# Kernel tuning notes

Hardware: AMD Instinct MI355X
Metric: run time of the kernel (lower is better)

Reference implementation:

```python
import jax, jax.numpy as jnp
import numpy as np

GROUPS = 32
EPS = 1e-6


def group_norm(x, gamma, beta):
    # x: [B, C, T], normalize per group of channels over (C//G, T)
    B, C, T = x.shape
    xr = x.reshape(B, GROUPS, C // GROUPS, T)
    mean = xr.mean(axis=(2, 3), keepdims=True)
    var = xr.var(axis=(2, 3), keepdims=True)
    xn = ((xr - mean) * jax.lax.rsqrt(var + EPS)).reshape(B, C, T)
    return xn * gamma[None, :, None] + beta[None, :, None]


def conv1x1(h, w, b):
    # 1x1 Conv1d == channel matmul. h: [B,C,T], w: [O,C], b: [O]
    return jnp.einsum('oc,bct->bot', w, h) + b[None, :, None]


def setup_inputs() -> dict:
    key = jax.random.key(0)
    ks = jax.random.split(key, 10)
    B, C, T = 8, 512, 2048
    s = 1.0 / np.sqrt(C)
    return {
        'x': jax.random.normal(ks[0], (B, C, T), jnp.float32),
        'gamma': jnp.ones((C,), jnp.float32),
        'beta': jnp.zeros((C,), jnp.float32),
        'q_w': jax.random.normal(ks[1], (C, C), jnp.float32) * s,
        'q_b': jnp.zeros((C,), jnp.float32),
        'k_w': jax.random.normal(ks[2], (C, C), jnp.float32) * s,
        'k_b': jnp.zeros((C,), jnp.float32),
        'v_w': jax.random.normal(ks[3], (C, C), jnp.float32) * s,
        'v_b': jnp.zeros((C,), jnp.float32),
        'o_w': jax.random.normal(ks[4], (C, C), jnp.float32) * s,
        'o_b': jnp.zeros((C,), jnp.float32),
    }


def reference(x, gamma, beta, q_w, q_b, k_w, k_b, v_w, v_b, o_w, o_b):
    h = group_norm(x, gamma, beta)
    q = conv1x1(h, q_w, q_b)  # [B,C,T]
    k = conv1x1(h, k_w, k_b)
    v = conv1x1(h, v_w, v_b)
    B, C, T = q.shape
    scale = jnp.asarray(C, q.dtype) ** -0.5
    # scores[b,t,s] = sum_c q[b,c,t] * k[b,c,s]
    scores = jnp.einsum('bct,bcs->bts', q, k) * scale
    w = jax.nn.softmax(scores, axis=-1)
    # out[b,c,t] = sum_s v[b,c,s] * w[b,t,s]
    h = jnp.einsum('bcs,bts->bct', v, w)
    h = conv1x1(h, o_w, o_b)
    return x + h
```

## Files before the change

kernel.cpp:

```cpp
#include <hip/hip_runtime.h>
#include <hip/hip_bf16.h>
#include <stdint.h>

typedef __bf16 bf16_t;
typedef __attribute__((ext_vector_type(8))) __bf16 bf16x8;
typedef __attribute__((ext_vector_type(4))) __bf16 bf16x4;
typedef __attribute__((ext_vector_type(4))) float f32x4;

__device__ __forceinline__ bool is_fp32(const void* gamma) {
  return ((const unsigned*)gamma)[0] == 0x3F800000u;
}

__device__ __forceinline__ void async_copy16(const bf16_t* g, bf16_t* l) {
  __builtin_amdgcn_global_load_lds(
      (const __attribute__((address_space(1))) void*)g,
      (__attribute__((address_space(3))) void*)l, 16, 0, 0);
}

#define GFENCE() asm volatile("" ::: "memory")

__device__ __forceinline__ void hard_barrier() {
  GFENCE();
  __builtin_amdgcn_sched_barrier(0);
  __builtin_amdgcn_s_barrier();
  __builtin_amdgcn_sched_barrier(0);
  GFENCE();
}

template <int NW>
__device__ __forceinline__ void vm_wait() {
  if constexpr (NW == 8)
    asm volatile("s_waitcnt vmcnt(8)" ::: "memory");
  else if constexpr (NW == 6)
    asm volatile("s_waitcnt vmcnt(6)" ::: "memory");
  else
    asm volatile("s_waitcnt vmcnt(0)" ::: "memory");
}

__global__ __launch_bounds__(256) void prepass(
    const void* __restrict__ q_w, const void* __restrict__ k_w,
    const void* __restrict__ v_w, const void* __restrict__ o_w,
    const void* __restrict__ gamma, const void* __restrict__ beta,
    const void* __restrict__ q_b, const void* __restrict__ k_b,
    const void* __restrict__ v_b, const void* __restrict__ o_b,
    const void* __restrict__ xv, bf16_t* __restrict__ wdst,
    bf16_t* __restrict__ vdst, float* __restrict__ rowsum,
    float* __restrict__ stats) {
  const bool fp32 = is_fp32(gamma);
  int bid = blockIdx.x;
  int tid = threadIdx.x;
  if (bid < 4172) {
    int i = bid * 256 + tid;
    if (i < 1048576) {
      const void* wsrc[4] = {q_w, k_w, v_w, o_w};
      int seg = i >> 18, off = i & 262143;
      const void* s = wsrc[seg];
      wdst[i] = fp32 ? (bf16_t)((const float*)s)[off] : ((const bf16_t*)s)[off];
    } else {
      int j = i - 1048576;
      if (j < 3072) {
        const void* vsrc[6] = {gamma, beta, q_b, k_b, v_b, o_b};
        int seg = j >> 9, off = j & 511;
        const void* s = vsrc[seg];
        vdst[j] =
            fp32 ? (bf16_t)((const float*)s)[off] : ((const bf16_t*)s)[off];
      } else {
        int j2 = j - 3072;
        if (j2 < 16384) rowsum[j2] = 0.0f;
      }
    }
    return;
  }
  int gidx = bid - 4172;
  long long base = (long long)gidx * 16 * 2048;
  float s = 0.f, q = 0.f;
#pragma unroll
  for (int ch = 0; ch < 16; ++ch) {
    long long off = base + (long long)ch * 2048 + tid * 8;
    float f[8];
    if (fp32) {
      const float* xf = (const float*)xv;
      float4 u = *(const float4*)(xf + off);
      float4 w = *(const float4*)(xf + off + 4);
      f[0] = u.x; f[1] = u.y; f[2] = u.z; f[3] = u.w;
      f[4] = w.x; f[5] = w.y; f[6] = w.z; f[7] = w.w;
    } else {
      bf16x8 vv = *(const bf16x8*)((const bf16_t*)xv + off);
#pragma unroll
      for (int e = 0; e < 8; ++e) f[e] = (float)vv[e];
    }
#pragma unroll
    for (int e = 0; e < 8; ++e) {
      s += f[e];
      q += f[e] * f[e];
    }
  }
  for (int o = 32; o > 0; o >>= 1) {
    s += __shfl_down(s, o);
    q += __shfl_down(q, o);
  }
  __shared__ float red[8];
  int wave = tid >> 6, lane = tid & 63;
  if (lane == 0) {
    red[wave] = s;
    red[4 + wave] = q;
  }
  __syncthreads();
  if (tid == 0) {
    stats[gidx * 2 + 0] = red[0] + red[1] + red[2] + red[3];
    stats[gidx * 2 + 1] = red[4] + red[5] + red[6] + red[7];
  }
}

__global__ __launch_bounds__(256) void gn_apply(const void* __restrict__ xv,
                                                const float* __restrict__ stats,
                                                const bf16_t* __restrict__ gammab,
                                                const bf16_t* __restrict__ betab,
                                                bf16_t* __restrict__ ht,
                                                const void* __restrict__ gamma) {
  const int C = 512, T = 2048;
  const bool fp32 = is_fp32(gamma);
  int bid = blockIdx.x;
  int ts = bid & 3;
  int gp = (bid >> 2) & 15;
  int b = bid >> 6;
  int tid = threadIdx.x;
  int c0 = gp * 32;
  int t0 = ts * 512;
  int cw = tid & 31;
  int gloc = cw >> 4;
  int gidx = b * 32 + gp * 2 + gloc;
  const float inv = 1.0f / 32768.0f;
  float mean = stats[gidx * 2] * inv;
  float var = stats[gidx * 2 + 1] * inv - mean * mean;
  float rstd = rsqrtf(var + 1e-6f);
  float sc = rstd * (float)gammab[c0 + cw];
  float sh = (float)betab[c0 + cw] - mean * sc;

  __shared__ bf16_t tile[32 * 68];
  const float* xf = (const float*)xv;
  const bf16_t* xb = (const bf16_t*)xv;
  long long xbase = ((long long)b * C + c0) * T + t0;
  bf16_t* hb = ht + ((long long)b * T + t0) * C + c0;
  for (int ch = 0; ch < 8; ++ch) {
    if (fp32) {
#pragma unroll
      for (int p = 0; p < 2; ++p) {
        int e = p * 256 + tid;
        int c = e >> 4, t = (e & 15) * 4;
        long long off = xbase + (long long)c * T + ch * 64 + t;
        float4 u = *(const float4*)(xf + off);
        bf16x4 w;
        w[0] = (bf16_t)u.x; w[1] = (bf16_t)u.y;
        w[2] = (bf16_t)u.z; w[3] = (bf16_t)u.w;
        *(bf16x4*)&tile[c * 68 + t] = w;
      }
    } else {
      int c = tid >> 3, t = (tid & 7) * 8;
      long long off = xbase + (long long)c * T + ch * 64 + t;
      bf16x8 u = *(const bf16x8*)(xb + off);
      bf16x4 lo, hi;
#pragma unroll
      for (int e = 0; e < 4; ++e) { lo[e] = u[e]; hi[e] = u[e + 4]; }
      *(bf16x4*)&tile[c * 68 + t] = lo;
      *(bf16x4*)&tile[c * 68 + t + 4] = hi;
    }
    __syncthreads();
#pragma unroll
    for (int s2 = 0; s2 < 8; ++s2) {
      int t = s2 * 8 + (tid >> 5);
      float v = (float)tile[cw * 68 + t];
      hb[(long long)(ch * 64 + t) * C + cw] = (bf16_t)(v * sc + sh);
    }
    __syncthreads();
  }
}

template <int BM, bool BIASM, bool BIASN, bool RESOUT, bool EXPSUM,
          bool NORMROW, int M, int N, int K, int LDA, int LDB, int LDC>
__device__ __forceinline__ void gemm8_body(
    const bf16_t* __restrict__ A, long long sA, const bf16_t* __restrict__ B,
    long long sB, void* __restrict__ Cout, long long sC,
    const bf16_t* __restrict__ biasM, const bf16_t* __restrict__ biasN,
    const void* __restrict__ Res, long long sR, float alpha,
    const void* __restrict__ gamma, float* __restrict__ rowsum, int m0, int n0,
    int b, bf16_t* lds) {
  constexpr int AI = BM / 32;
  constexpr int AR = BM * 32;
  constexpr int L = BM / 128 + 2;
  const int tid = threadIdx.x;
  const int lane = tid & 63;
  const int lane15 = lane & 15;
  const int quad = lane >> 4;
  const int wave = tid >> 6;
  const int wm = wave >> 2;
  const int wn = wave & 3;

  const bf16_t* Ab = A + (long long)b * sA + (long long)m0 * LDA;
  const bf16_t* Bb = B + (long long)b * sB + (long long)n0 * LDB;

  bf16_t* ldsA = lds;
  bf16_t* ldsB = lds + 4 * AR;

  const int srow = tid >> 2;
  const int sg = ((tid & 3) - (srow >> 1)) & 3;
  const bf16_t* As_src = Ab + (long long)srow * LDA + sg * 8;
  const bf16_t* Bs_src = Bb + (long long)srow * LDB + sg * 8;
  const long long A128 = 128LL * LDA, B128 = 128LL * LDB;

  auto stA = [&](int kelem, int r) {
    async_copy16(As_src + kelem, ldsA + r * AR + tid * 8);
    if constexpr (BM == 256)
      async_copy16(As_src + A128 + kelem, ldsA + r * AR + tid * 8 + 4096);
  };
  auto stB = [&](int kelem, int r) {
    async_copy16(Bs_src + kelem, ldsB + r * 8192 + tid * 8);
    async_copy16(Bs_src + B128 + kelem, ldsB + r * 8192 + tid * 8 + 4096);
  };

  const int slot = ((quad + (lane15 >> 1)) & 3) * 8;
  const int aoff = (wm * (BM / 2) + lane15) * 32 + slot;
  const int boff = (wn * 64 + lane15) * 32 + slot;

  bf16x8 af[AI];
  f32x4 acc[AI][4] = {};

  auto lda_frags = [&](int r) {
#pragma unroll
    for (int i = 0; i < AI; ++i)
      af[i] = *(const bf16x8*)(ldsA + r * AR + aoff + i * 512);
  };
  auto ldbf = [&](int r, int j) {
    return *(const bf16x8*)(ldsB + r * 8192 + boff + j * 512);
  };

  auto phaseA = [&](int rdA, int rdB, int stk, int str) {
    lda_frags(rdA);
    bf16x8 b0 = ldbf(rdB, 0), b1 = ldbf(rdB, 1);
    stA(stk, str);
    hard_barrier();
    asm volatile("s_waitcnt lgkmcnt(0)" ::: "memory");
    __builtin_amdgcn_sched_barrier(0);
    __builtin_amdgcn_s_setprio(1);
#pragma unroll
    for (int i = 0; i < AI; ++i) {
      acc[i][0] = __builtin_amdgcn_mfma_f32_16x16x32_bf16(af[i], b0, acc[i][0], 0, 0, 0);
      acc[i][1] = __builtin_amdgcn_mfma_f32_16x16x32_bf16(af[i], b1, acc[i][1], 0, 0, 0);
    }
    __builtin_amdgcn_s_setprio(0);
    hard_barrier();
  };
  auto phaseB = [&](int rdB, int stk, int str) {
    bf16x8 b0 = ldbf(rdB, 2), b1 = ldbf(rdB, 3);
    stB(stk, str);
    hard_barrier();
    asm volatile("s_waitcnt lgkmcnt(0)" ::: "memory");
    __builtin_amdgcn_sched_barrier(0);
    __builtin_amdgcn_s_setprio(1);
#pragma unroll
    for (int i = 0; i < AI; ++i) {
      acc[i][2] = __builtin_amdgcn_mfma_f32_16x16x32_bf16(af[i], b0, acc[i][2], 0, 0, 0);
      acc[i][3] = __builtin_amdgcn_mfma_f32_16x16x32_bf16(af[i], b1, acc[i][3], 0, 0, 0);
    }
    __builtin_amdgcn_s_setprio(0);
    vm_wait<2 * L>();
    hard_barrier();
  };

  const int NT = K / 64;
  const int NI = NT / 2;

  stA(0, 0);
  stB(0, 0);
  stA(32, 1);
  stB(32, 1);
  stA(64, 2);
  stB(64, 2);
  vm_wait<2 * L>();
  hard_barrier();

#pragma unroll 1
  for (int it = 0; it < NI; ++it) {
    const int ku = it * 128;
    const bool last = (it == NI - 1);
    const int ku2 = last ? 0 : ku + 128;
    const int kv2 = last ? 64 : ku + 192;
    phaseA(0, 0, ku + 96, 3);
    phaseB(0, ku + 96, 3);
    phaseA(1, 1, ku2, 0);
    phaseB(1, ku2, 0);
    phaseA(2, 2, ku2 + 32, 1);
    phaseB(2, ku2 + 32, 1);
    phaseA(3, 3, kv2, 2);
    phaseB(3, kv2, 2);
  }
  asm volatile("s_waitcnt vmcnt(0)" ::: "memory");

  if (EXPSUM) {
#pragma unroll
    for (int i = 0; i < AI; ++i) {
#pragma unroll
      for (int r = 0; r < 4; ++r) {
        long long m = m0 + wm * (BM / 2) + i * 16 + quad * 4 + r;
        float partial = 0.f;
#pragma unroll
        for (int j = 0; j < 4; ++j) {
          long long n = n0 + wn * 64 + j * 16 + lane15;
          float v = __expf(acc[i][j][r] * alpha);
          partial += v;
          ((bf16_t*)Cout)[(long long)b * sC + m * LDC + n] = (bf16_t)v;
        }
        partial += __shfl_xor(partial, 1);
        partial += __shfl_xor(partial, 2);
        partial += __shfl_xor(partial, 4);
        partial += __shfl_xor(partial, 8);
        if (lane15 == 0) atomicAdd(&rowsum[(long long)b * M + m], partial);
      }
    }
    return;
  }

  float invr[AI][4];
  if (NORMROW) {
#pragma unroll
    for (int i = 0; i < AI; ++i)
#pragma unroll
      for (int r = 0; r < 4; ++r)
        invr[i][r] = 1.0f / rowsum[(long long)b * M + m0 + wm * (BM / 2) +
                                   i * 16 + quad * 4 + r];
  }
  bool fp32 = false;
  if (RESOUT) fp32 = is_fp32(gamma);
#pragma unroll
  for (int i = 0; i < AI; ++i) {
#pragma unroll
    for (int j = 0; j < 4; ++j) {
#pragma unroll
      for (int r = 0; r < 4; ++r) {
        long long m = m0 + wm * (BM / 2) + i * 16 + quad * 4 + r;
        long long n = n0 + wn * 64 + j * 16 + lane15;
        float v = acc[i][j][r] * alpha;
        if (NORMROW) v *= invr[i][r];
        if (BIASM) v += (float)biasM[m];
        if (BIASN) v += (float)biasN[n];
        long long idx = (long long)b * sC + m * LDC + n;
        if (RESOUT) {
          long long ridx = (long long)b * sR + m * LDC + n;
          if (fp32) {
            v += ((const float*)Res)[ridx];
            ((float*)Cout)[idx] = v;
          } else {
            v += (float)((const bf16_t*)Res)[ridx];
            ((bf16_t*)Cout)[idx] = (bf16_t)v;
          }
        } else {
          ((bf16_t*)Cout)[idx] = (bf16_t)v;
        }
      }
    }
  }
}

__global__ __launch_bounds__(512, 2) void qkv_fat(
    const bf16_t* __restrict__ ht, const bf16_t* __restrict__ wqk,
    const bf16_t* __restrict__ wv, bf16_t* __restrict__ qkt,
    bf16_t* __restrict__ vvb, const bf16_t* __restrict__ qkb,
    const bf16_t* __restrict__ vbb, const void* __restrict__ gamma) {
  __shared__ __align__(16) bf16_t lds[65536];
  const long long TC = 2048LL * 512, CT = 512LL * 2048;
  int bid = blockIdx.x;
  if (bid < 256) {
    int b = bid >> 5, rem = bid & 31;
    int n0 = (rem & 3) * 256, m0 = (rem >> 2) * 256;
    gemm8_body<256, false, true, false, false, false, 2048, 1024, 512, 512,
               512, 1024>(ht, TC, wqk, 0, qkt, 2048LL * 1024, nullptr, qkb,
                          nullptr, 0, 1.0f, gamma, nullptr, m0, n0, b, lds);
  } else {
    int id2 = bid - 256;
    int b = id2 >> 5, rem = id2 & 31;
    int m0 = (rem & 3) * 128, n0 = (rem >> 2) * 256;
    gemm8_body<128, true, false, false, false, false, 512, 2048, 512, 512,
               512, 2048>(wv, 0, ht, TC, vvb, CT, vbb, nullptr, nullptr, 0,
                          1.0f, gamma, nullptr, m0, n0, b, lds);
  }
}

__global__ __launch_bounds__(512, 2) void scores_kernel(
    const bf16_t* __restrict__ qkt, bf16_t* __restrict__ Sm,
    const void* __restrict__ gamma, float* __restrict__ rowsum, float alpha) {
  __shared__ __align__(16) bf16_t lds[65536];
  int x = blockIdx.x;
  int gid = x >> 4, win = x & 15;
  int gm = gid & 1, gn = gid >> 1;
  int m0 = (gm * 4 + (win & 3)) * 256;
  int n0 = (gn * 4 + (win >> 2)) * 256;
  gemm8_body<256, false, false, false, true, false, 2048, 2048, 512, 1024,
             1024, 2048>(qkt, 2048LL * 1024, qkt + 512, 2048LL * 1024, Sm,
                         2048LL * 2048, nullptr, nullptr, nullptr, 0, alpha,
                         gamma, rowsum, m0, n0, blockIdx.z, lds);
}

__global__ __launch_bounds__(512, 2) void av_kernel(
    const bf16_t* __restrict__ Sm, const bf16_t* __restrict__ vvb,
    bf16_t* __restrict__ h2t, const void* __restrict__ gamma,
    float* __restrict__ rowsum) {
  __shared__ __align__(16) bf16_t lds[49152];
  gemm8_body<128, false, false, false, false, true, 2048, 512, 2048, 2048,
             2048, 512>(Sm, 2048LL * 2048, vvb, 512LL * 2048, h2t,
                        2048LL * 512, nullptr, nullptr, nullptr, 0, 1.0f,
                        gamma, rowsum, blockIdx.y * 128, blockIdx.x * 256,
                        blockIdx.z, lds);
}

__global__ __launch_bounds__(512, 2) void final_kernel(
    const bf16_t* __restrict__ wo, const bf16_t* __restrict__ h2t,
    void* __restrict__ out, const bf16_t* __restrict__ obb,
    const void* __restrict__ x, const void* __restrict__ gamma) {
  __shared__ __align__(16) bf16_t lds[49152];
  const long long TC = 2048LL * 512, CT = 512LL * 2048;
  gemm8_body<128, true, false, true, false, false, 512, 2048, 512, 512, 512,
             2048>(wo, 0, h2t, TC, out, CT, obb, nullptr, x, CT, 1.0f, gamma,
                   nullptr, blockIdx.y * 128, blockIdx.x * 256, blockIdx.z,
                   lds);
}

extern "C" void kernel_launch(void* const* d_in, const int* in_sizes, int n_in,
                              void* d_out, int out_size, void* d_ws,
                              size_t ws_size, hipStream_t stream) {
  const void* x = d_in[0];
  const void* gamma = d_in[1];
  const void* beta = d_in[2];
  const void* q_w = d_in[3];
  const void* q_b = d_in[4];
  const void* k_w = d_in[5];
  const void* k_b = d_in[6];
  const void* v_w = d_in[7];
  const void* v_b = d_in[8];
  const void* o_w = d_in[9];
  const void* o_b = d_in[10];

  const long long BTC = 8LL * 2048 * 512;
  char* ws = (char*)d_ws;
  float* stats = (float*)(ws + 256);
  bf16_t* wq = (bf16_t*)(ws + 4096);
  bf16_t* wv = wq + 2 * 262144;
  bf16_t* wo = wq + 3 * 262144;
  bf16_t* vdst = wq + 4 * 262144;
  bf16_t* gammab = vdst + 0 * 512;
  bf16_t* betab = vdst + 1 * 512;
  bf16_t* qkb = vdst + 2 * 512;
  bf16_t* vbb = vdst + 4 * 512;
  bf16_t* obb = vdst + 5 * 512;
  float* rowsum = (float*)(ws + 4096 + 2 * 1024 * 1024 + 8192);
  const size_t hdr = 4096 + 2 * 1024 * 1024 + 8192 + 65536;
  bf16_t* ht = (bf16_t*)(ws + hdr);
  bf16_t* vvb = ht + BTC;
  bf16_t* Sm = vvb + BTC;
  bf16_t* h2t = ht;
  bf16_t* qkt = (bf16_t*)d_out;

  const float scale = 0.044194173824159216f;

  prepass<<<4428, 256, 0, stream>>>(q_w, k_w, v_w, o_w, gamma, beta, q_b, k_b,
                                    v_b, o_b, x, wq, vdst, rowsum, stats);
  gn_apply<<<512, 256, 0, stream>>>(x, stats, gammab, betab, ht, gamma);
  qkv_fat<<<512, 512, 0, stream>>>(ht, wq, wv, qkt, vvb, qkb, vbb, gamma);
  scores_kernel<<<dim3(64, 1, 8), 512, 0, stream>>>(qkt, Sm, gamma, rowsum,
                                                    scale);
  av_kernel<<<dim3(2, 16, 8), 512, 0, stream>>>(Sm, vvb, h2t, gamma, rowsum);
  final_kernel<<<dim3(8, 4, 8), 512, 0, stream>>>(wo, h2t, d_out, obb, x,
                                                  gamma);
}
```

Measured before the change: 279.9 us.

## Fuse all stages into one cooperative persistent kernel with grid syncs

Replaces the six separate kernel launches with a single cooperative kernel of 256 blocks that runs prepass, group-norm apply, QKV, scores, AV and output projection as stages separated by grid.sync, with a multi-launch fallback. The GEMM body now loops over several tiles per block and prefetches the next tile's first k-slices during the last iteration, so one persistent block can cover more work. This removes launch gaps and tail effects between kernels. In exchange it fixes the grid at 256 blocks (about one per CU), which lowers occupancy, and it adds grid-wide barrier costs.

```diff
diff --git a/kernel.cpp b/kernel.cpp
--- a/kernel.cpp
+++ b/kernel.cpp
@@ -1,6 +1,9 @@
 #include <hip/hip_runtime.h>
+#include <hip/hip_cooperative_groups.h>
 #include <hip/hip_bf16.h>
 #include <stdint.h>
+
+namespace cg = cooperative_groups;
 
 typedef __bf16 bf16_t;
 typedef __attribute__((ext_vector_type(8))) __bf16 bf16x8;
@@ -37,154 +40,15 @@
     asm volatile("s_waitcnt vmcnt(0)" ::: "memory");
 }
 
-__global__ __launch_bounds__(256) void prepass(
-    const void* __restrict__ q_w, const void* __restrict__ k_w,
-    const void* __restrict__ v_w, const void* __restrict__ o_w,
-    const void* __restrict__ gamma, const void* __restrict__ beta,
-    const void* __restrict__ q_b, const void* __restrict__ k_b,
-    const void* __restrict__ v_b, const void* __restrict__ o_b,
-    const void* __restrict__ xv, bf16_t* __restrict__ wdst,
-    bf16_t* __restrict__ vdst, float* __restrict__ rowsum,
-    float* __restrict__ stats) {
-  const bool fp32 = is_fp32(gamma);
-  int bid = blockIdx.x;
-  int tid = threadIdx.x;
-  if (bid < 4172) {
-    int i = bid * 256 + tid;
-    if (i < 1048576) {
-      const void* wsrc[4] = {q_w, k_w, v_w, o_w};
-      int seg = i >> 18, off = i & 262143;
-      const void* s = wsrc[seg];
-      wdst[i] = fp32 ? (bf16_t)((const float*)s)[off] : ((const bf16_t*)s)[off];
-    } else {
-      int j = i - 1048576;
-      if (j < 3072) {
-        const void* vsrc[6] = {gamma, beta, q_b, k_b, v_b, o_b};
-        int seg = j >> 9, off = j & 511;
-        const void* s = vsrc[seg];
-        vdst[j] =
-            fp32 ? (bf16_t)((const float*)s)[off] : ((const bf16_t*)s)[off];
-      } else {
-        int j2 = j - 3072;
-        if (j2 < 16384) rowsum[j2] = 0.0f;
-      }
-    }
-    return;
-  }
-  int gidx = bid - 4172;
-  long long base = (long long)gidx * 16 * 2048;
-  float s = 0.f, q = 0.f;
-#pragma unroll
-  for (int ch = 0; ch < 16; ++ch) {
-    long long off = base + (long long)ch * 2048 + tid * 8;
-    float f[8];
-    if (fp32) {
-      const float* xf = (const float*)xv;
-      float4 u = *(const float4*)(xf + off);
-      float4 w = *(const float4*)(xf + off + 4);
-      f[0] = u.x; f[1] = u.y; f[2] = u.z; f[3] = u.w;
-      f[4] = w.x; f[5] = w.y; f[6] = w.z; f[7] = w.w;
-    } else {
-      bf16x8 vv = *(const bf16x8*)((const bf16_t*)xv + off);
-#pragma unroll
-      for (int e = 0; e < 8; ++e) f[e] = (float)vv[e];
-    }
-#pragma unroll
-    for (int e = 0; e < 8; ++e) {
-      s += f[e];
-      q += f[e] * f[e];
-    }
-  }
-  for (int o = 32; o > 0; o >>= 1) {
-    s += __shfl_down(s, o);
-    q += __shfl_down(q, o);
-  }
-  __shared__ float red[8];
-  int wave = tid >> 6, lane = tid & 63;
-  if (lane == 0) {
-    red[wave] = s;
-    red[4 + wave] = q;
-  }
-  __syncthreads();
-  if (tid == 0) {
-    stats[gidx * 2 + 0] = red[0] + red[1] + red[2] + red[3];
-    stats[gidx * 2 + 1] = red[4] + red[5] + red[6] + red[7];
-  }
-}
-
-__global__ __launch_bounds__(256) void gn_apply(const void* __restrict__ xv,
-                                                const float* __restrict__ stats,
-                                                const bf16_t* __restrict__ gammab,
-                                                const bf16_t* __restrict__ betab,
-                                                bf16_t* __restrict__ ht,
-                                                const void* __restrict__ gamma) {
-  const int C = 512, T = 2048;
-  const bool fp32 = is_fp32(gamma);
-  int bid = blockIdx.x;
-  int ts = bid & 3;
-  int gp = (bid >> 2) & 15;
-  int b = bid >> 6;
-  int tid = threadIdx.x;
-  int c0 = gp * 32;
-  int t0 = ts * 512;
-  int cw = tid & 31;
-  int gloc = cw >> 4;
-  int gidx = b * 32 + gp * 2 + gloc;
-  const float inv = 1.0f / 32768.0f;
-  float mean = stats[gidx * 2] * inv;
-  float var = stats[gidx * 2 + 1] * inv - mean * mean;
-  float rstd = rsqrtf(var + 1e-6f);
-  float sc = rstd * (float)gammab[c0 + cw];
-  float sh = (float)betab[c0 + cw] - mean * sc;
-
-  __shared__ bf16_t tile[32 * 68];
-  const float* xf = (const float*)xv;
-  const bf16_t* xb = (const bf16_t*)xv;
-  long long xbase = ((long long)b * C + c0) * T + t0;
-  bf16_t* hb = ht + ((long long)b * T + t0) * C + c0;
-  for (int ch = 0; ch < 8; ++ch) {
-    if (fp32) {
-#pragma unroll
-      for (int p = 0; p < 2; ++p) {
-        int e = p * 256 + tid;
-        int c = e >> 4, t = (e & 15) * 4;
-        long long off = xbase + (long long)c * T + ch * 64 + t;
-        float4 u = *(const float4*)(xf + off);
-        bf16x4 w;
-        w[0] = (bf16_t)u.x; w[1] = (bf16_t)u.y;
-        w[2] = (bf16_t)u.z; w[3] = (bf16_t)u.w;
-        *(bf16x4*)&tile[c * 68 + t] = w;
-      }
-    } else {
-      int c = tid >> 3, t = (tid & 7) * 8;
-      long long off = xbase + (long long)c * T + ch * 64 + t;
-      bf16x8 u = *(const bf16x8*)(xb + off);
-      bf16x4 lo, hi;
-#pragma unroll
-      for (int e = 0; e < 4; ++e) { lo[e] = u[e]; hi[e] = u[e + 4]; }
-      *(bf16x4*)&tile[c * 68 + t] = lo;
-      *(bf16x4*)&tile[c * 68 + t + 4] = hi;
-    }
-    __syncthreads();
-#pragma unroll
-    for (int s2 = 0; s2 < 8; ++s2) {
-      int t = s2 * 8 + (tid >> 5);
-      float v = (float)tile[cw * 68 + t];
-      hb[(long long)(ch * 64 + t) * C + cw] = (bf16_t)(v * sc + sh);
-    }
-    __syncthreads();
-  }
-}
-
-template <int BM, bool BIASM, bool BIASN, bool RESOUT, bool EXPSUM,
+template <int BM, int TCNT, bool BIASM, bool BIASN, bool RESOUT, bool EXPSUM,
           bool NORMROW, int M, int N, int K, int LDA, int LDB, int LDC>
 __device__ __forceinline__ void gemm8_body(
     const bf16_t* __restrict__ A, long long sA, const bf16_t* __restrict__ B,
     long long sB, void* __restrict__ Cout, long long sC,
     const bf16_t* __restrict__ biasM, const bf16_t* __restrict__ biasN,
     const void* __restrict__ Res, long long sR, float alpha,
-    const void* __restrict__ gamma, float* __restrict__ rowsum, int m0, int n0,
-    int b, bf16_t* lds) {
+    const void* __restrict__ gamma, float* __restrict__ rowsum,
+    const int* m0s, const int* n0s, int b, bf16_t* lds) {
   constexpr int AI = BM / 32;
   constexpr int AR = BM * 32;
   constexpr int L = BM / 128 + 2;
@@ -196,26 +60,21 @@
   const int wm = wave >> 2;
   const int wn = wave & 3;
 
-  const bf16_t* Ab = A + (long long)b * sA + (long long)m0 * LDA;
-  const bf16_t* Bb = B + (long long)b * sB + (long long)n0 * LDB;
-
   bf16_t* ldsA = lds;
   bf16_t* ldsB = lds + 4 * AR;
 
   const int srow = tid >> 2;
   const int sg = ((tid & 3) - (srow >> 1)) & 3;
-  const bf16_t* As_src = Ab + (long long)srow * LDA + sg * 8;
-  const bf16_t* Bs_src = Bb + (long long)srow * LDB + sg * 8;
   const long long A128 = 128LL * LDA, B128 = 128LL * LDB;
 
-  auto stA = [&](int kelem, int r) {
-    async_copy16(As_src + kelem, ldsA + r * AR + tid * 8);
+  auto stA = [&](const bf16_t* src, int kelem, int r) {
+    async_copy16(src + kelem, ldsA + r * AR + tid * 8);
     if constexpr (BM == 256)
-      async_copy16(As_src + A128 + kelem, ldsA + r * AR + tid * 8 + 4096);
+      async_copy16(src + A128 + kelem, ldsA + r * AR + tid * 8 + 4096);
   };
-  auto stB = [&](int kelem, int r) {
-    async_copy16(Bs_src + kelem, ldsB + r * 8192 + tid * 8);
-    async_copy16(Bs_src + B128 + kelem, ldsB + r * 8192 + tid * 8 + 4096);
+  auto stB = [&](const bf16_t* src, int kelem, int r) {
+    async_copy16(src + kelem, ldsB + r * 8192 + tid * 8);
+    async_copy16(src + B128 + kelem, ldsB + r * 8192 + tid * 8 + 4096);
   };
 
   const int slot = ((quad + (lane15 >> 1)) & 3) * 8;
@@ -223,7 +82,7 @@
   const int boff = (wn * 64 + lane15) * 32 + slot;
 
   bf16x8 af[AI];
-  f32x4 acc[AI][4] = {};
+  f32x4 acc[AI][4];
 
   auto lda_frags = [&](int r) {
 #pragma unroll
@@ -234,10 +93,10 @@
     return *(const bf16x8*)(ldsB + r * 8192 + boff + j * 512);
   };
 
-  auto phaseA = [&](int rdA, int rdB, int stk, int str) {
+  auto phaseA = [&](int rdA, int rdB, const bf16_t* src, int stk, int str) {
     lda_frags(rdA);
     bf16x8 b0 = ldbf(rdB, 0), b1 = ldbf(rdB, 1);
-    stA(stk, str);
+    stA(src, stk, str);
     hard_barrier();
     asm volatile("s_waitcnt lgkmcnt(0)" ::: "memory");
     __builtin_amdgcn_sched_barrier(0);
@@ -250,9 +109,9 @@
     __builtin_amdgcn_s_setprio(0);
     hard_barrier();
   };
-  auto phaseB = [&](int rdB, int stk, int str) {
+  auto phaseB = [&](int rdB, const bf16_t* src, int stk, int str) {
     bf16x8 b0 = ldbf(rdB, 2), b1 = ldbf(rdB, 3);
-    stB(stk, str);
+    stB(src, stk, str);
     hard_barrier();
     asm volatile("s_waitcnt lgkmcnt(0)" ::: "memory");
     __builtin_amdgcn_sched_barrier(0);
@@ -267,161 +126,386 @@
     hard_barrier();
   };
 
-  const int NT = K / 64;
-  const int NI = NT / 2;
-
-  stA(0, 0);
-  stB(0, 0);
-  stA(32, 1);
-  stB(32, 1);
-  stA(64, 2);
-  stB(64, 2);
-  vm_wait<2 * L>();
-  hard_barrier();
+  constexpr int NI = K / 128;
+
+#pragma unroll
+  for (int t = 0; t < TCNT; ++t) {
+    const int m0 = m0s[t], n0 = n0s[t];
+    const bf16_t* Acur = A + (long long)b * sA + (long long)m0 * LDA +
+                         (long long)srow * LDA + sg * 8;
+    const bf16_t* Bcur = B + (long long)b * sB + (long long)n0 * LDB +
+                         (long long)srow * LDB + sg * 8;
+    const int tn = (t + 1 < TCNT) ? t + 1 : t;
+    const bf16_t* Anxt = A + (long long)b * sA + (long long)m0s[tn] * LDA +
+                         (long long)srow * LDA + sg * 8;
+    const bf16_t* Bnxt = B + (long long)b * sB + (long long)n0s[tn] * LDB +
+                         (long long)srow * LDB + sg * 8;
+
+    if (t == 0) {
+      stA(Acur, 0, 0); stB(Bcur, 0, 0);
+      stA(Acur, 32, 1); stB(Bcur, 32, 1);
+      stA(Acur, 64, 2); stB(Bcur, 64, 2);
+      vm_wait<2 * L>();
+      hard_barrier();
+    }
+
+#pragma unroll
+    for (int i = 0; i < AI; ++i)
+#pragma unroll
+      for (int j = 0; j < 4; ++j) acc[i][j] = {0.f, 0.f, 0.f, 0.f};
 
 #pragma unroll 1
-  for (int it = 0; it < NI; ++it) {
-    const int ku = it * 128;
-    const bool last = (it == NI - 1);
-    const int ku2 = last ? 0 : ku + 128;
-    const int kv2 = last ? 64 : ku + 192;
-    phaseA(0, 0, ku + 96, 3);
-    phaseB(0, ku + 96, 3);
-    phaseA(1, 1, ku2, 0);
-    phaseB(1, ku2, 0);
-    phaseA(2, 2, ku2 + 32, 1);
-    phaseB(2, ku2 + 32, 1);
-    phaseA(3, 3, kv2, 2);
-    phaseB(3, kv2, 2);
-  }
-  asm volatile("s_waitcnt vmcnt(0)" ::: "memory");
-
-  if (EXPSUM) {
-#pragma unroll
-    for (int i = 0; i < AI; ++i) {
-#pragma unroll
-      for (int r = 0; r < 4; ++r) {
-        long long m = m0 + wm * (BM / 2) + i * 16 + quad * 4 + r;
-        float partial = 0.f;
-#pragma unroll
-        for (int j = 0; j < 4; ++j) {
-          long long n = n0 + wn * 64 + j * 16 + lane15;
-          float v = __expf(acc[i][j][r] * alpha);
-          partial += v;
-          ((bf16_t*)Cout)[(long long)b * sC + m * LDC + n] = (bf16_t)v;
-        }
-        partial += __shfl_xor(partial, 1);
-        partial += __shfl_xor(partial, 2);
-        partial += __shfl_xor(partial, 4);
-        partial += __shfl_xor(partial, 8);
-        if (lane15 == 0) atomicAdd(&rowsum[(long long)b * M + m], partial);
-      }
-    }
-    return;
-  }
-
-  float invr[AI][4];
-  if (NORMROW) {
-#pragma unroll
-    for (int i = 0; i < AI; ++i)
-#pragma unroll
-      for (int r = 0; r < 4; ++r)
-        invr[i][r] = 1.0f / rowsum[(long long)b * M + m0 + wm * (BM / 2) +
-                                   i * 16 + quad * 4 + r];
-  }
-  bool fp32 = false;
-  if (RESOUT) fp32 = is_fp32(gamma);
-#pragma unroll
-  for (int i = 0; i < AI; ++i) {
-#pragma unroll
-    for (int j = 0; j < 4; ++j) {
-#pragma unroll
-      for (int r = 0; r < 4; ++r) {
-        long long m = m0 + wm * (BM / 2) + i * 16 + quad * 4 + r;
-        long long n = n0 + wn * 64 + j * 16 + lane15;
-        float v = acc[i][j][r] * alpha;
-        if (NORMROW) v *= invr[i][r];
-        if (BIASM) v += (float)biasM[m];
-        if (BIASN) v += (float)biasN[n];
-        long long idx = (long long)b * sC + m * LDC + n;
-        if (RESOUT) {
-          long long ridx = (long long)b * sR + m * LDC + n;
-          if (fp32) {
-            v += ((const float*)Res)[ridx];
-            ((float*)Cout)[idx] = v;
-          } else {
-            v += (float)((const bf16_t*)Res)[ridx];
-            ((bf16_t*)Cout)[idx] = (bf16_t)v;
+    for (int it = 0; it < NI; ++it) {
+      const int ku = it * 128;
+      const bool lastit = (it == NI - 1);
+      const bf16_t* sAs = lastit ? Anxt : Acur;
+      const bf16_t* sBs = lastit ? Bnxt : Bcur;
+      const int k0n = lastit ? 0 : ku + 128;
+      const int k1n = lastit ? 32 : ku + 160;
+      const int k2n = lastit ? 64 : ku + 192;
+      phaseA(0, 0, Acur, ku + 96, 3);
+      phaseB(0, Bcur, ku + 96, 3);
+      phaseA(1, 1, sAs, k0n, 0);
+      phaseB(1, sBs, k0n, 0);
+      phaseA(2, 2, sAs, k1n, 1);
+      phaseB(2, sBs, k1n, 1);
+      phaseA(3, 3, sAs, k2n, 2);
+      phaseB(3, sBs, k2n, 2);
+    }
+    if (t == TCNT - 1) asm volatile("s_waitcnt vmcnt(0)" ::: "memory");
+
+    if constexpr (EXPSUM) {
+#pragma unroll
+      for (int i = 0; i < AI; ++i) {
+#pragma unroll
+        for (int r = 0; r < 4; ++r) {
+          long long m = m0 + wm * (BM / 2) + i * 16 + quad * 4 + r;
+          float partial = 0.f;
+#pragma unroll
+          for (int j = 0; j < 4; ++j) {
+            long long n = n0 + wn * 64 + j * 16 + lane15;
+            float v = __expf(acc[i][j][r] * alpha);
+            partial += v;
+            ((bf16_t*)Cout)[(long long)b * sC + m * LDC + n] = (bf16_t)v;
           }
-        } else {
-          ((bf16_t*)Cout)[idx] = (bf16_t)v;
+          partial += __shfl_xor(partial, 1);
+          partial += __shfl_xor(partial, 2);
+          partial += __shfl_xor(partial, 4);
+          partial += __shfl_xor(partial, 8);
+          if (lane15 == 0) atomicAdd(&rowsum[(long long)b * M + m], partial);
         }
       }
-    }
-  }
-}
-
-__global__ __launch_bounds__(512, 2) void qkv_fat(
-    const bf16_t* __restrict__ ht, const bf16_t* __restrict__ wqk,
-    const bf16_t* __restrict__ wv, bf16_t* __restrict__ qkt,
-    bf16_t* __restrict__ vvb, const bf16_t* __restrict__ qkb,
-    const bf16_t* __restrict__ vbb, const void* __restrict__ gamma) {
-  __shared__ __align__(16) bf16_t lds[65536];
+    } else {
+      float invr[AI][4];
+      if constexpr (NORMROW) {
+#pragma unroll
+        for (int i = 0; i < AI; ++i)
+#pragma unroll
+          for (int r = 0; r < 4; ++r)
+            invr[i][r] = 1.0f / rowsum[(long long)b * M + m0 + wm * (BM / 2) +
+                                       i * 16 + quad * 4 + r];
+      }
+      bool f32o = false;
+      if constexpr (RESOUT) f32o = is_fp32(gamma);
+#pragma unroll
+      for (int i = 0; i < AI; ++i) {
+#pragma unroll
+        for (int j = 0; j < 4; ++j) {
+#pragma unroll
+          for (int r = 0; r < 4; ++r) {
+            long long m = m0 + wm * (BM / 2) + i * 16 + quad * 4 + r;
+            long long n = n0 + wn * 64 + j * 16 + lane15;
+            float v = acc[i][j][r] * alpha;
+            if constexpr (NORMROW) v *= invr[i][r];
+            if constexpr (BIASM) v += (float)biasM[m];
+            if constexpr (BIASN) v += (float)biasN[n];
+            long long idx = (long long)b * sC + m * LDC + n;
+            if constexpr (RESOUT) {
+              long long ridx = (long long)b * sR + m * LDC + n;
+              if (f32o) {
+                v += ((const float*)Res)[ridx];
+                ((float*)Cout)[idx] = v;
+              } else {
+                v += (float)((const bf16_t*)Res)[ridx];
+                ((bf16_t*)Cout)[idx] = (bf16_t)v;
+              }
+            } else {
+              ((bf16_t*)Cout)[idx] = (bf16_t)v;
+            }
+          }
+        }
+      }
+    }
+  }
+}
+
+__device__ __forceinline__ void stage_prepass(
+    int bid, const void* __restrict__ xv, const void* __restrict__ gamma,
+    const void* __restrict__ beta, const void* __restrict__ q_w,
+    const void* __restrict__ q_b, const void* __restrict__ k_w,
+    const void* __restrict__ k_b, const void* __restrict__ v_w,
+    const void* __restrict__ v_b, const void* __restrict__ o_w,
+    const void* __restrict__ o_b, bf16_t* __restrict__ wdst,
+    float* __restrict__ rowsum, float* __restrict__ stats, bf16_t* lds) {
+  const bool fp32 = is_fp32(gamma);
+  const int tid = threadIdx.x;
+  bf16_t* vdst = wdst + 4 * 262144;
+  {
+    int i = (bid * 512 + tid) * 8;
+    const void* wsrc[4] = {q_w, k_w, v_w, o_w};
+    int seg = i >> 18, off = i & 262143;
+    const void* s = wsrc[seg];
+    bf16x8 w8;
+    if (fp32) {
+      const float* sf = (const float*)s + off;
+      float4 u = *(const float4*)sf;
+      float4 w = *(const float4*)(sf + 4);
+      w8[0] = (bf16_t)u.x; w8[1] = (bf16_t)u.y;
+      w8[2] = (bf16_t)u.z; w8[3] = (bf16_t)u.w;
+      w8[4] = (bf16_t)w.x; w8[5] = (bf16_t)w.y;
+      w8[6] = (bf16_t)w.z; w8[7] = (bf16_t)w.w;
+    } else {
+      w8 = *(const bf16x8*)((const bf16_t*)s + off);
+    }
+    *(bf16x8*)(wdst + i) = w8;
+  }
+  if (bid == 0) {
+    const void* vsrc[6] = {gamma, beta, q_b, k_b, v_b, o_b};
+#pragma unroll
+    for (int rep = 0; rep < 6; ++rep) {
+      int j = rep * 512 + tid;
+      const void* s2 = vsrc[rep];
+      vdst[j] = fp32 ? (bf16_t)((const float*)s2)[tid]
+                     : ((const bf16_t*)s2)[tid];
+    }
+  }
+  if (bid >= 8 && bid < 16) {
+    float4 z = {0.f, 0.f, 0.f, 0.f};
+    *(float4*)(rowsum + (((bid - 8) << 9) + tid) * 4) = z;
+  }
+  long long base = (long long)bid * 16 * 2048;
+  float s1 = 0.f, s2 = 0.f;
+#pragma unroll
+  for (int ch = 0; ch < 16; ++ch) {
+    long long off = base + ch * 2048 + tid * 4;
+    float f[4];
+    if (fp32) {
+      float4 u = *(const float4*)((const float*)xv + off);
+      f[0] = u.x; f[1] = u.y; f[2] = u.z; f[3] = u.w;
+    } else {
+      bf16x4 u = *(const bf16x4*)((const bf16_t*)xv + off);
+#pragma unroll
+      for (int e = 0; e < 4; ++e) f[e] = (float)u[e];
+    }
+#pragma unroll
+    for (int e = 0; e < 4; ++e) { s1 += f[e]; s2 += f[e] * f[e]; }
+  }
+  for (int o = 32; o > 0; o >>= 1) {
+    s1 += __shfl_down(s1, o);
+    s2 += __shfl_down(s2, o);
+  }
+  float* red = (float*)lds;
+  int wv_ = tid >> 6, ln = tid & 63;
+  if (ln == 0) { red[wv_] = s1; red[8 + wv_] = s2; }
+  __syncthreads();
+  if (tid == 0) {
+    float a = 0.f, c = 0.f;
+#pragma unroll
+    for (int w = 0; w < 8; ++w) { a += red[w]; c += red[8 + w]; }
+    stats[bid * 2] = a;
+    stats[bid * 2 + 1] = c;
+  }
+  __syncthreads();
+}
+
+__device__ __forceinline__ void stage_gn_one(
+    int vb, const void* __restrict__ xv, const float* __restrict__ stats,
+    const bf16_t* __restrict__ wdst, bf16_t* __restrict__ ht,
+    const void* __restrict__ gamma, bf16_t* lds) {
+  const int C = 512, T = 2048;
+  const bool fp32 = is_fp32(gamma);
+  const bf16_t* vdst = wdst + 4 * 262144;
+  const bf16_t* gammab = vdst;
+  const bf16_t* betab = vdst + 512;
+  int ts = vb & 3, gp = (vb >> 2) & 15, b = vb >> 6;
+  int tid = threadIdx.x;
+  int c0 = gp * 32, t0 = ts * 512;
+  int cw = tid & 31;
+  int gidx = b * 32 + gp * 2 + (cw >> 4);
+  const float inv = 1.0f / 32768.0f;
+  float mean = stats[gidx * 2] * inv;
+  float var = stats[gidx * 2 + 1] * inv - mean * mean;
+  float rstd = rsqrtf(var + 1e-6f);
+  float sc = rstd * (float)gammab[c0 + cw];
+  float sh = (float)betab[c0 + cw] - mean * sc;
+
+  bf16_t* tile = lds;
+  const float* xf = (const float*)xv;
+  const bf16_t* xb = (const bf16_t*)xv;
+  long long xbase = ((long long)b * C + c0) * T + t0;
+  bf16_t* hb = ht + ((long long)b * T + t0) * C + c0;
+  for (int ch = 0; ch < 8; ++ch) {
+    {
+      int c = tid >> 4, t = (tid & 15) * 4;
+      long long off = xbase + (long long)c * T + ch * 64 + t;
+      bf16x4 w;
+      if (fp32) {
+        float4 u = *(const float4*)(xf + off);
+        w[0] = (bf16_t)u.x; w[1] = (bf16_t)u.y;
+        w[2] = (bf16_t)u.z; w[3] = (bf16_t)u.w;
+      } else {
+        w = *(const bf16x4*)(xb + off);
+      }
+      *(bf16x4*)&tile[c * 68 + t] = w;
+    }
+    __syncthreads();
+#pragma unroll
+    for (int s2 = 0; s2 < 4; ++s2) {
+      int t = s2 * 16 + (tid >> 5);
+      float v = (float)tile[cw * 68 + t];
+      hb[(long long)(ch * 64 + t) * C + cw] = (bf16_t)(v * sc + sh);
+    }
+    __syncthreads();
+  }
+}
+
+__device__ __forceinline__ void stage_qkv(int bid, const bf16_t* ht,
+                                          const bf16_t* wdst, bf16_t* qkt,
+                                          bf16_t* vvb, const void* gamma,
+                                          bf16_t* lds) {
   const long long TC = 2048LL * 512, CT = 512LL * 2048;
-  int bid = blockIdx.x;
-  if (bid < 256) {
-    int b = bid >> 5, rem = bid & 31;
-    int n0 = (rem & 3) * 256, m0 = (rem >> 2) * 256;
-    gemm8_body<256, false, true, false, false, false, 2048, 1024, 512, 512,
-               512, 1024>(ht, TC, wqk, 0, qkt, 2048LL * 1024, nullptr, qkb,
-                          nullptr, 0, 1.0f, gamma, nullptr, m0, n0, b, lds);
-  } else {
-    int id2 = bid - 256;
-    int b = id2 >> 5, rem = id2 & 31;
-    int m0 = (rem & 3) * 128, n0 = (rem >> 2) * 256;
-    gemm8_body<128, true, false, false, false, false, 512, 2048, 512, 512,
+  const bf16_t* vdst = wdst + 4 * 262144;
+  const bf16_t* qkb = vdst + 1024;
+  const bf16_t* vbb = vdst + 2048;
+  const bf16_t* wv = wdst + 2 * 262144;
+  int b = bid >> 5, rem = bid & 31;
+  {
+    int m0s[1] = {(rem >> 2) * 256}, n0s[1] = {(rem & 3) * 256};
+    gemm8_body<256, 1, false, true, false, false, false, 2048, 1024, 512, 512,
+               512, 1024>(ht, TC, wdst, 0, qkt, 2048LL * 1024, nullptr, qkb,
+                          nullptr, 0, 1.0f, gamma, nullptr, m0s, n0s, b, lds);
+  }
+  {
+    int m0s[1] = {(rem & 3) * 128}, n0s[1] = {(rem >> 2) * 256};
+    gemm8_body<128, 1, true, false, false, false, false, 512, 2048, 512, 512,
                512, 2048>(wv, 0, ht, TC, vvb, CT, vbb, nullptr, nullptr, 0,
-                          1.0f, gamma, nullptr, m0, n0, b, lds);
-  }
-}
-
-__global__ __launch_bounds__(512, 2) void scores_kernel(
-    const bf16_t* __restrict__ qkt, bf16_t* __restrict__ Sm,
-    const void* __restrict__ gamma, float* __restrict__ rowsum, float alpha) {
-  __shared__ __align__(16) bf16_t lds[65536];
-  int x = blockIdx.x;
-  int gid = x >> 4, win = x & 15;
-  int gm = gid & 1, gn = gid >> 1;
-  int m0 = (gm * 4 + (win & 3)) * 256;
-  int n0 = (gn * 4 + (win >> 2)) * 256;
-  gemm8_body<256, false, false, false, true, false, 2048, 2048, 512, 1024,
+                          1.0f, gamma, nullptr, m0s, n0s, b, lds);
+  }
+}
+
+__device__ __forceinline__ void stage_scores(int bid, const bf16_t* qkt,
+                                             bf16_t* Sm, const void* gamma,
+                                             float* rowsum, bf16_t* lds) {
+  int b = bid >> 5, xx = bid & 31;
+  int n0 = (xx >> 2) * 256, mq = xx & 3;
+  int m0s[2] = {mq * 256, (mq + 4) * 256};
+  int n0s[2] = {n0, n0};
+  gemm8_body<256, 2, false, false, false, true, false, 2048, 2048, 512, 1024,
              1024, 2048>(qkt, 2048LL * 1024, qkt + 512, 2048LL * 1024, Sm,
-                         2048LL * 2048, nullptr, nullptr, nullptr, 0, alpha,
-                         gamma, rowsum, m0, n0, blockIdx.z, lds);
-}
-
-__global__ __launch_bounds__(512, 2) void av_kernel(
-    const bf16_t* __restrict__ Sm, const bf16_t* __restrict__ vvb,
-    bf16_t* __restrict__ h2t, const void* __restrict__ gamma,
-    float* __restrict__ rowsum) {
-  __shared__ __align__(16) bf16_t lds[49152];
-  gemm8_body<128, false, false, false, false, true, 2048, 512, 2048, 2048,
+                         2048LL * 2048, nullptr, nullptr, nullptr, 0,
+                         0.044194173824159216f, gamma, rowsum, m0s, n0s, b,
+                         lds);
+}
+
+__device__ __forceinline__ void stage_av(int bid, const bf16_t* Sm,
+                                         const bf16_t* vvb, bf16_t* h2t,
+                                         const void* gamma, float* rowsum,
+                                         bf16_t* lds) {
+  int b = bid >> 5, rem = bid & 31;
+  int m0s[1] = {(rem >> 1) * 128}, n0s[1] = {(rem & 1) * 256};
+  gemm8_body<128, 1, false, false, false, false, true, 2048, 512, 2048, 2048,
              2048, 512>(Sm, 2048LL * 2048, vvb, 512LL * 2048, h2t,
                         2048LL * 512, nullptr, nullptr, nullptr, 0, 1.0f,
-                        gamma, rowsum, blockIdx.y * 128, blockIdx.x * 256,
-                        blockIdx.z, lds);
-}
-
-__global__ __launch_bounds__(512, 2) void final_kernel(
-    const bf16_t* __restrict__ wo, const bf16_t* __restrict__ h2t,
-    void* __restrict__ out, const bf16_t* __restrict__ obb,
-    const void* __restrict__ x, const void* __restrict__ gamma) {
-  __shared__ __align__(16) bf16_t lds[49152];
-  const long long TC = 2048LL * 512, CT = 512LL * 2048;
-  gemm8_body<128, true, false, true, false, false, 512, 2048, 512, 512, 512,
-             2048>(wo, 0, h2t, TC, out, CT, obb, nullptr, x, CT, 1.0f, gamma,
-                   nullptr, blockIdx.y * 128, blockIdx.x * 256, blockIdx.z,
-                   lds);
+                        gamma, rowsum, m0s, n0s, b, lds);
+}
+
+__device__ __forceinline__ void stage_final(int bid, const bf16_t* wdst,
+                                            const bf16_t* h2t, void* outp,
+                                            const void* x, const void* gamma,
+                                            bf16_t* lds) {
+  const bf16_t* vdst = wdst + 4 * 262144;
+  const bf16_t* obb = vdst + 2560;
+  const bf16_t* wo = wdst + 3 * 262144;
+  int b = bid >> 5, rem = bid & 31;
+  int m0s[1] = {(rem & 3) * 128}, n0s[1] = {(rem >> 2) * 256};
+  gemm8_body<128, 1, true, false, true, false, false, 512, 2048, 512, 512,
+             512, 2048>(wo, 0, h2t, 2048LL * 512, outp, 512LL * 2048, obb,
+                        nullptr, x, 512LL * 2048, 1.0f, gamma, nullptr, m0s,
+                        n0s, b, lds);
+}
+
+__global__ __launch_bounds__(512, 2) void mega(
+    const void* __restrict__ x, const void* __restrict__ gamma,
+    const void* __restrict__ beta, const void* __restrict__ q_w,
+    const void* __restrict__ q_b, const void* __restrict__ k_w,
+    const void* __restrict__ k_b, const void* __restrict__ v_w,
+    const void* __restrict__ v_b, const void* __restrict__ o_w,
+    const void* __restrict__ o_b, bf16_t* __restrict__ wdst,
+    float* __restrict__ stats, float* __restrict__ rowsum,
+    bf16_t* __restrict__ ht, bf16_t* __restrict__ vvb,
+    bf16_t* __restrict__ Sm, bf16_t* __restrict__ qkt,
+    void* __restrict__ outp) {
+  __shared__ __align__(16) bf16_t lds[65536];
+  cg::grid_group grid = cg::this_grid();
+  const int bid = blockIdx.x;
+  stage_prepass(bid, x, gamma, beta, q_w, q_b, k_w, k_b, v_w, v_b, o_w, o_b,
+                wdst, rowsum, stats, lds);
+  grid.sync();
+  stage_gn_one(bid, x, stats, wdst, ht, gamma, lds);
+  stage_gn_one(256 + bid, x, stats, wdst, ht, gamma, lds);
+  grid.sync();
+  stage_qkv(bid, ht, wdst, qkt, vvb, gamma, lds);
+  grid.sync();
+  stage_scores(bid, qkt, Sm, gamma, rowsum, lds);
+  grid.sync();
+  stage_av(bid, Sm, vvb, ht, gamma, rowsum, lds);
+  grid.sync();
+  stage_final(bid, wdst, ht, outp, x, gamma, lds);
+}
+
+__global__ __launch_bounds__(512, 2) void k_prepass(
+    const void* x, const void* gamma, const void* beta, const void* q_w,
+    const void* q_b, const void* k_w, const void* k_b, const void* v_w,
+    const void* v_b, const void* o_w, const void* o_b, bf16_t* wdst,
+    float* rowsum, float* stats) {
+  __shared__ __align__(16) bf16_t lds[65536];
+  stage_prepass(blockIdx.x, x, gamma, beta, q_w, q_b, k_w, k_b, v_w, v_b, o_w,
+                o_b, wdst, rowsum, stats, lds);
+}
+__global__ __launch_bounds__(512, 2) void k_gn(const void* x,
+                                               const float* stats,
+                                               const bf16_t* wdst, bf16_t* ht,
+                                               const void* gamma) {
+  __shared__ __align__(16) bf16_t lds[65536];
+  stage_gn_one(blockIdx.x, x, stats, wdst, ht, gamma, lds);
+}
+__global__ __launch_bounds__(512, 2) void k_qkv(const bf16_t* ht,
+                                                const bf16_t* wdst,
+                                                bf16_t* qkt, bf16_t* vvb,
+                                                const void* gamma) {
+  __shared__ __align__(16) bf16_t lds[65536];
+  stage_qkv(blockIdx.x, ht, wdst, qkt, vvb, gamma, lds);
+}
+__global__ __launch_bounds__(512, 2) void k_scores(const bf16_t* qkt,
+                                                   bf16_t* Sm,
+                                                   const void* gamma,
+                                                   float* rowsum) {
+  __shared__ __align__(16) bf16_t lds[65536];
+  stage_scores(blockIdx.x, qkt, Sm, gamma, rowsum, lds);
+}
+__global__ __launch_bounds__(512, 2) void k_av(const bf16_t* Sm,
+                                               const bf16_t* vvb, bf16_t* h2t,
+                                               const void* gamma,
+                                               float* rowsum) {
+  __shared__ __align__(16) bf16_t lds[65536];
+  stage_av(blockIdx.x, Sm, vvb, h2t, gamma, rowsum, lds);
+}
+__global__ __launch_bounds__(512, 2) void k_final(const bf16_t* wdst,
+                                                  const bf16_t* h2t,
+                                                  void* outp, const void* x,
+                                                  const void* gamma) {
+  __shared__ __align__(16) bf16_t lds[65536];
+  stage_final(blockIdx.x, wdst, h2t, outp, x, gamma, lds);
 }
 
 extern "C" void kernel_launch(void* const* d_in, const int* in_sizes, int n_in,
@@ -442,32 +526,30 @@
   const long long BTC = 8LL * 2048 * 512;
   char* ws = (char*)d_ws;
   float* stats = (float*)(ws + 256);
-  bf16_t* wq = (bf16_t*)(ws + 4096);
-  bf16_t* wv = wq + 2 * 262144;
-  bf16_t* wo = wq + 3 * 262144;
-  bf16_t* vdst = wq + 4 * 262144;
-  bf16_t* gammab = vdst + 0 * 512;
-  bf16_t* betab = vdst + 1 * 512;
-  bf16_t* qkb = vdst + 2 * 512;
-  bf16_t* vbb = vdst + 4 * 512;
-  bf16_t* obb = vdst + 5 * 512;
+  bf16_t* wdst = (bf16_t*)(ws + 4096);
   float* rowsum = (float*)(ws + 4096 + 2 * 1024 * 1024 + 8192);
   const size_t hdr = 4096 + 2 * 1024 * 1024 + 8192 + 65536;
   bf16_t* ht = (bf16_t*)(ws + hdr);
   bf16_t* vvb = ht + BTC;
   bf16_t* Sm = vvb + BTC;
-  bf16_t* h2t = ht;
   bf16_t* qkt = (bf16_t*)d_out;
-
-  const float scale = 0.044194173824159216f;
-
-  prepass<<<4428, 256, 0, stream>>>(q_w, k_w, v_w, o_w, gamma, beta, q_b, k_b,
-                                    v_b, o_b, x, wq, vdst, rowsum, stats);
-  gn_apply<<<512, 256, 0, stream>>>(x, stats, gammab, betab, ht, gamma);
-  qkv_fat<<<512, 512, 0, stream>>>(ht, wq, wv, qkt, vvb, qkb, vbb, gamma);
-  scores_kernel<<<dim3(64, 1, 8), 512, 0, stream>>>(qkt, Sm, gamma, rowsum,
-                                                    scale);
-  av_kernel<<<dim3(2, 16, 8), 512, 0, stream>>>(Sm, vvb, h2t, gamma, rowsum);
-  final_kernel<<<dim3(8, 4, 8), 512, 0, stream>>>(wo, h2t, d_out, obb, x,
-                                                  gamma);
-}
+  void* outp = d_out;
+
+  void* args[] = {(void*)&x,     (void*)&gamma, (void*)&beta, (void*)&q_w,
+                  (void*)&q_b,   (void*)&k_w,   (void*)&k_b,  (void*)&v_w,
+                  (void*)&v_b,   (void*)&o_w,   (void*)&o_b,  (void*)&wdst,
+                  (void*)&stats, (void*)&rowsum, (void*)&ht,  (void*)&vvb,
+                  (void*)&Sm,    (void*)&qkt,   (void*)&outp};
+  hipError_t err = hipLaunchCooperativeKernel((void*)mega, dim3(256),
+                                              dim3(512), args, 0, stream);
+  if (err != hipSuccess) {
+    k_prepass<<<256, 512, 0, stream>>>(x, gamma, beta, q_w, q_b, k_w, k_b,
+                                       v_w, v_b, o_w, o_b, wdst, rowsum,
+                                       stats);
+    k_gn<<<512, 512, 0, stream>>>(x, stats, wdst, ht, gamma);
+    k_qkv<<<256, 512, 0, stream>>>(ht, wdst, qkt, vvb, gamma);
+    k_scores<<<256, 512, 0, stream>>>(qkt, Sm, gamma, rowsum);
+    k_av<<<256, 512, 0, stream>>>(Sm, vvb, ht, gamma, rowsum);
+    k_final<<<256, 512, 0, stream>>>(wdst, ht, outp, x, gamma);
+  }
+}
```

Result: slower. 461.8 us (+65.0%).
